# Kernel tuning notes

Hardware: AMD Instinct MI355X
Metric: run time of the kernel (lower is better)

Reference implementation:

```python
import jax, jax.numpy as jnp
import numpy as np
from jax import lax

EPS = 1e-5
DN = ('NCHW', 'OIHW', 'NCHW')


def _bn(x, gamma, beta, mean, var):
    # eval-mode BatchNorm2d over channel dim (axis=1)
    s = gamma / jnp.sqrt(var + EPS)
    return x * s[None, :, None, None] + (beta - mean * s)[None, :, None, None]


def setup_inputs() -> dict:
    key = jax.random.key(0)
    ks = jax.random.split(key, 12)
    B, Cin, C, H, W, NC = 128, 2048, 512, 14, 14, 200
    return {
        'feature': jax.random.normal(ks[0], (B, Cin, H, W), jnp.float32),
        'w_reduce': jax.random.normal(ks[1], (C, Cin, 1, 1), jnp.float32) * 0.02,
        'b_reduce': jax.random.normal(ks[2], (C,), jnp.float32) * 0.02,
        'bn1_gamma': jnp.ones((C,), jnp.float32),
        'bn1_beta': jnp.zeros((C,), jnp.float32),
        'bn1_mean': jax.random.normal(ks[3], (C,), jnp.float32) * 0.02,
        'bn1_var': jax.random.uniform(ks[4], (C,), jnp.float32),
        'w3': jax.random.normal(ks[5], (C, C, 3, 3), jnp.float32) * 0.02,
        'b3': jax.random.normal(ks[6], (C,), jnp.float32) * 0.02,
        'bn2_gamma': jnp.ones((C,), jnp.float32),
        'bn2_beta': jnp.zeros((C,), jnp.float32),
        'bn2_mean': jax.random.normal(ks[7], (C,), jnp.float32) * 0.02,
        'bn2_var': jax.random.uniform(ks[8], (C,), jnp.float32),
        'fc1_w': jax.random.normal(ks[9], (NC, C), jnp.float32) * 0.02,
        'fc1_b': jnp.zeros((NC,), jnp.float32),
        'fc2_w': jax.random.normal(ks[10], (NC, NC), jnp.float32) * 0.02,
        'fc2_b': jnp.zeros((NC,), jnp.float32),
    }


def reference(feature, w_reduce, b_reduce, bn1_gamma, bn1_beta, bn1_mean, bn1_var,
              w3, b3, bn2_gamma, bn2_beta, bn2_mean, bn2_var,
              fc1_w, fc1_b, fc2_w, fc2_b):
    B, _, H, W = feature.shape
    C = w_reduce.shape[0]  # 512
    # reduce: 1x1 conv + BN + ReLU
    f = lax.conv_general_dilated(feature, w_reduce, (1, 1), 'VALID', dimension_numbers=DN)
    f = f + b_reduce[None, :, None, None]
    f = jax.nn.relu(_bn(f, bn1_gamma, bn1_beta, bn1_mean, bn1_var))
    x = f.reshape(B, C, H * W)  # [B, 512, 196]
    # channel affinity + softmax(-xxt) over last dim (= the per-row loop)
    xxt = jnp.einsum('bcn,bdn->bcd', x, x)  # [B, 512, 512]
    a = jax.nn.softmax(-xxt, axis=2)
    y = jnp.einsum('bcd,bdn->bcn', a, x).reshape(B, C, H, W)
    # conv3: 3x3 conv + BN + ReLU + global avg pool
    z = lax.conv_general_dilated(y, w3, (1, 1), 'SAME', dimension_numbers=DN)
    z = z + b3[None, :, None, None]
    z = jax.nn.relu(_bn(z, bn2_gamma, bn2_beta, bn2_mean, bn2_var))
    z = jnp.mean(z, axis=(2, 3))  # [B, 512]
    # fc_channel: Linear -> ReLU -> Linear
    h = jax.nn.relu(z @ fc1_w.T + fc1_b)
    sf = h @ fc2_w.T + fc2_b
    return sf
```

## Files before the change

kernel.cpp:

```cpp
#include <hip/hip_runtime.h>

typedef __attribute__((ext_vector_type(8))) short bf16x8;
typedef __attribute__((ext_vector_type(4))) float f32x4;
typedef __attribute__((ext_vector_type(4))) short short4v;
typedef __attribute__((ext_vector_type(2))) short short2v;

__device__ __forceinline__ unsigned short f2bf(float x){
  unsigned u = __float_as_uint(x);
  return (unsigned short)((u + 0x7FFFu + ((u>>16)&1u)) >> 16);
}
__device__ __forceinline__ float bf2f(unsigned short b){
  return __uint_as_float(((unsigned)b)<<16);
}

typedef const __attribute__((address_space(1))) void* gas_t;
typedef __attribute__((address_space(3))) void* las_t;
__device__ __forceinline__ void gl16(const void* g, void* l){
  __builtin_amdgcn_global_load_lds((gas_t)g, (las_t)l, 16, 0, 0);
}

static constexpr size_t O_FHI  = 0;
static constexpr size_t O_FLO  = 102760448;
static constexpr size_t O_XHI  = 205520896;
static constexpr size_t O_XLO  = 239075328;
static constexpr size_t O_XT   = 272629760;
static constexpr size_t O_AMAT = 301989888;
static constexpr size_t O_WH   = 369098752;
static constexpr size_t O_WL   = 371195904;
static constexpr size_t O_W3B  = 373293056;
static constexpr size_t O_PAR  = 378011648;
static constexpr size_t O_FC1T = 378019840;
static constexpr size_t O_FC2T = 378429440;
static constexpr size_t O_ZBAR = 378589440;

__global__ __launch_bounds__(256) void k_prep(
    const float* wr, unsigned short* wh, unsigned short* wl,
    const float* w3, unsigned short* w3c,
    const float* fc1w, float* fc1T, const float* fc2w, float* fc2T,
    const float* br, const float* g1, const float* be1, const float* m1, const float* v1,
    const float* b3, const float* g2, const float* be2, const float* m2, const float* v2,
    float* par, unsigned short* xhi, unsigned short* xlo){
  int blk = blockIdx.x, t = threadIdx.x;
  if (blk < 4096){
    int idx = blk*256 + t;
    int c = idx >> 11, k = idx & 2047;
    float v = wr[(size_t)c*2048 + k];
    unsigned short h = f2bf(v);
    wh[(size_t)c*2048+k] = h; wl[(size_t)c*2048+k] = f2bf(v - bf2f(h));
  } else if (blk < 13312){
    int i = (blk-4096)*256 + t;
    int co = i / 4608, k = i - co*4608;
    int ci0b = k / 576, r2 = k - ci0b*576;
    int tap = r2 >> 6, cio = r2 & 63;
    w3c[(((size_t)ci0b*9+tap)*512+co)*64+cio] =
        f2bf(w3[((size_t)co*512 + ci0b*64+cio)*9 + tap]);
  } else if (blk < 13712){
    int i = (blk-13312)*256 + t;
    int k = i/200, j = i - k*200;
    fc1T[i] = fc1w[j*512+k];
  } else if (blk < 13869){
    int i = (blk-13712)*256 + t;
    if (i < 40000){ int k = i/200, j = i - k*200; fc2T[i] = fc2w[j*200+k]; }
  } else if (blk < 13871){
    int c = (blk-13869)*256 + t;
    if (c < 512){
      float s1 = g1[c]*rsqrtf(v1[c]+1e-5f);
      par[c] = s1; par[512+c] = (br[c]-m1[c])*s1 + be1[c];
      float s2 = g2[c]*rsqrtf(v2[c]+1e-5f);
      par[1024+c] = s2; par[1536+c] = (b3[c]-m2[c])*s2 + be2[c];
    }
  } else {
    int rr = (blk-13871)*256 + t;
    float4 z = {0.f,0.f,0.f,0.f};
    float4* a = (float4*)(xhi + (size_t)rr*256 + 192);
    float4* bq = (float4*)(xlo + (size_t)rr*256 + 192);
    #pragma unroll
    for (int q=0;q<8;++q){ a[q]=z; bq[q]=z; }
  }
}

__global__ __launch_bounds__(256) void k_featT(const float* __restrict__ feat,
        unsigned short* __restrict__ fhi, unsigned short* __restrict__ flo){
  __shared__ float tile[64][33];
  int b = blockIdx.z;
  int ci0 = blockIdx.y*64, p0 = blockIdx.x*32;
  int t = threadIdx.x;
  int j = t & 31, i0 = t >> 5;
  for (int rep=0; rep<8; ++rep){
    int i = rep*8 + i0;
    int p = p0 + j;
    tile[i][j] = (p<196) ? feat[((size_t)b*2048 + ci0 + i)*196 + p] : 0.f;
  }
  __syncthreads();
  int j2 = t & 31;
  int jj0 = t >> 5;
  for (int rep=0; rep<4; ++rep){
    int jj = rep*8 + jj0;
    int p = p0 + jj;
    if (p < 196){
      float v0 = tile[2*j2][jj], v1 = tile[2*j2+1][jj];
      unsigned short h0 = f2bf(v0), h1 = f2bf(v1);
      unsigned short l0 = f2bf(v0 - bf2f(h0)), l1 = f2bf(v1 - bf2f(h1));
      size_t o = ((size_t)b*196 + p)*2048 + ci0 + 2*j2;
      short2v hv; hv[0]=(short)h0; hv[1]=(short)h1;
      short2v lv; lv[0]=(short)l0; lv[1]=(short)l1;
      *(short2v*)(fhi + o) = hv;
      *(short2v*)(flo + o) = lv;
    }
  }
}

__global__ __launch_bounds__(128, 1) void k_conv1(
    const unsigned short* __restrict__ fhi, const unsigned short* __restrict__ flo,
    const unsigned short* __restrict__ wh,  const unsigned short* __restrict__ wl,
    const float* __restrict__ par,
    unsigned short* __restrict__ xhi, unsigned short* __restrict__ xlo,
    unsigned short* __restrict__ xT){
  __shared__ char lds[65536];
  char* BUF0 = lds;
  char* BUF1 = lds + 32768;
  int lin = blockIdx.x;
  int sz  = (lin&7)*98 + (lin>>3);
  int mt = sz&3;
  int gt = sz>>2;
  int c0 = mt*128;
  size_t g0 = (size_t)gt*128;
  int t = threadIdx.x, lane = t&63, wv = t>>6;
  int fq = (lane>>4)&3, fr = lane&15;
  f32x4 acc[8][4] = {};

  auto STAGE = [&](int it, char* buf){
    #pragma unroll
    for (int jj=0; jj<16; ++jj){
      int arr = jj>>2;
      int g = (jj&3)*128 + t;
      int row = g>>2;
      int cs = ((g&3) ^ ((row>>1)&3))*8;
      const unsigned short* src;
      if (arr==0)      src = wh  + (size_t)(c0+row)*2048 + it*32 + cs;
      else if (arr==1) src = wl  + (size_t)(c0+row)*2048 + it*32 + cs;
      else if (arr==2) src = fhi + (g0+row)*2048 + it*32 + cs;
      else             src = flo + (g0+row)*2048 + it*32 + cs;
      gl16(src, buf + arr*8192 + g*16);
    }
  };

  STAGE(0, BUF0);
  asm volatile("s_waitcnt vmcnt(0)" ::: "memory");
  __builtin_amdgcn_s_barrier();
  __builtin_amdgcn_sched_barrier(0);

  for (int it=0; it<64; ++it){
    char* cur = (it&1) ? BUF1 : BUF0;
    char* nxt = (it&1) ? BUF0 : BUF1;
    if (it < 63) STAGE(it+1, nxt);
    bf16x8 ah[8], al[8];
    #pragma unroll
    for (int m=0;m<8;++m){
      int row = m*16 + fr;
      int off = row*64 + ((fq*16) ^ (((row>>1)&3)<<4));
      ah[m] = *(const bf16x8*)(cur + off);
      al[m] = *(const bf16x8*)(cur + 8192 + off);
    }
    __builtin_amdgcn_s_setprio(1);
    #pragma unroll
    for (int n=0;n<4;++n){
      int row = wv*64 + n*16 + fr;
      int off = row*64 + ((fq*16) ^ (((row>>1)&3)<<4));
      bf16x8 bh = *(const bf16x8*)(cur + 16384 + off);
      bf16x8 bl = *(const bf16x8*)(cur + 24576 + off);
      #pragma unroll
      for (int m=0;m<8;++m){
        acc[m][n] = __builtin_amdgcn_mfma_f32_16x16x32_bf16(ah[m], bh, acc[m][n],0,0,0);
        acc[m][n] = __builtin_amdgcn_mfma_f32_16x16x32_bf16(ah[m], bl, acc[m][n],0,0,0);
        acc[m][n] = __builtin_amdgcn_mfma_f32_16x16x32_bf16(al[m], bh, acc[m][n],0,0,0);
      }
    }
    __builtin_amdgcn_s_setprio(0);
    asm volatile("s_waitcnt vmcnt(0)" ::: "memory");
    __builtin_amdgcn_s_barrier();
    __builtin_amdgcn_sched_barrier(0);
  }

  const float* s1 = par; const float* t1 = par+512;
  for (int m=0;m<8;++m){
    int cb = c0 + m*16 + fq*4;
    float sc[4], sh[4];
    for (int j=0;j<4;++j){ sc[j]=s1[cb+j]; sh[j]=t1[cb+j]; }
    for (int n=0;n<4;++n){
      int gg = (int)g0 + wv*64 + n*16 + fr;
      int b = gg/196, p = gg - b*196;
      unsigned short hs[4];
      for (int j=0;j<4;++j){
        float v = fmaxf(acc[m][n][j]*sc[j]+sh[j], 0.f);
        unsigned short h = f2bf(v);
        hs[j] = h;
        size_t ic = (size_t)b*512 + cb + j;
        xhi[ic*256 + p] = h;
        xlo[ic*256 + p] = f2bf(v - bf2f(h));
      }
      *(short4v*)(xT + ((size_t)b*224 + p)*512 + cb) = *(short4v*)hs;
    }
  }
}

__global__ __launch_bounds__(256) void k_xxt(const unsigned short* __restrict__ xhi,
        const unsigned short* __restrict__ xlo, float* __restrict__ xxt){
  __shared__ char lds[32768];
  char* Als = lds; char* Bls = lds + 16384;
  int lin = blockIdx.x;
  int sz  = (lin&7)*160 + (lin>>3);
  int b = sz/10, sub = sz - b*10;
  unsigned mtp = (3u<<18)|(2u<<16)|(2u<<14)|(1u<<12)|(1u<<10)|(1u<<8)|(0u<<6)|(0u<<4)|(0u<<2)|0u;
  unsigned ntp = (3u<<18)|(3u<<16)|(2u<<14)|(3u<<12)|(2u<<10)|(1u<<8)|(3u<<6)|(2u<<4)|(1u<<2)|0u;
  int mt = (mtp>>(2*sub))&3, nt = (ntp>>(2*sub))&3;
  int c0 = mt*128, d0 = nt*128;
  int t = threadIdx.x, lane = t&63, wid = t>>6, wm = wid&1, wn = wid>>1;
  int fq = lane>>4, fr = lane&15;
  f32x4 acc[4][4] = {};
  for (int it=0; it<12; ++it){
    int seg = it>>2, kk0 = (it&3)*64;
    const unsigned short* As = (seg<2) ? xhi : xlo;
    const unsigned short* Bs = (seg==1) ? xlo : xhi;
    __syncthreads();
    #pragma unroll
    for (int r=0;r<4;++r){
      int L = r*256 + t;
      int row = L>>3, cs = ((L&7)^(row&7))*8;
      gl16(As + ((size_t)b*512 + c0 + row)*256 + kk0 + cs, Als + L*16);
      gl16(Bs + ((size_t)b*512 + d0 + row)*256 + kk0 + cs, Bls + L*16);
    }
    __syncthreads();
    #pragma unroll
    for (int ks=0; ks<2; ++ks){
      int kb = ks*64 + fq*16;
      bf16x8 af[4];
      #pragma unroll
      for (int m=0;m<4;++m){
        int row = wm*64 + m*16 + fr;
        af[m] = *(const bf16x8*)(Als + row*128 + (kb ^ ((row&7)<<4)));
      }
      #pragma unroll
      for (int n=0;n<4;++n){
        int row = wn*64 + n*16 + fr;
        bf16x8 bff = *(const bf16x8*)(Bls + row*128 + (kb ^ ((row&7)<<4)));
        #pragma unroll
        for (int m=0;m<4;++m)
          acc[m][n] = __builtin_amdgcn_mfma_f32_16x16x32_bf16(af[m], bff, acc[m][n],0,0,0);
      }
    }
  }
  for (int m=0;m<4;++m){
    int cb = c0 + wm*64 + m*16 + fq*4;
    for (int n=0;n<4;++n){
      int d = d0 + wn*64 + n*16 + fr;
      *(float4*)(xxt + ((size_t)b*512 + d)*512 + cb) = *(float4*)&acc[m][n];
    }
  }
  if (mt != nt){
    for (int m=0;m<4;++m){
      int cb = c0 + wm*64 + m*16 + fq*4;
      for (int n=0;n<4;++n){
        int d = d0 + wn*64 + n*16 + fr;
        for (int jj=0;jj<4;++jj)
          xxt[((size_t)b*512 + cb + jj)*512 + d] = acc[m][n][jj];
      }
    }
  }
}

__global__ __launch_bounds__(256) void k_softmax(const float* __restrict__ xxt, unsigned short* __restrict__ amat){
  int row = blockIdx.x*4 + (threadIdx.x>>6);
  int lane = threadIdx.x & 63;
  const float* src = xxt + (size_t)row*512 + lane*8;
  float4 v0 = *(const float4*)src;
  float4 v1 = *(const float4*)(src+4);
  float mn = fminf(fminf(fminf(v0.x,v0.y),fminf(v0.z,v0.w)),
                   fminf(fminf(v1.x,v1.y),fminf(v1.z,v1.w)));
  for (int m=32; m; m>>=1) mn = fminf(mn, __shfl_xor(mn, m, 64));
  float e[8];
  e[0]=__expf(mn-v0.x); e[1]=__expf(mn-v0.y); e[2]=__expf(mn-v0.z); e[3]=__expf(mn-v0.w);
  e[4]=__expf(mn-v1.x); e[5]=__expf(mn-v1.y); e[6]=__expf(mn-v1.z); e[7]=__expf(mn-v1.w);
  float s = e[0]+e[1]+e[2]+e[3]+e[4]+e[5]+e[6]+e[7];
  for (int m=32; m; m>>=1) s += __shfl_xor(s, m, 64);
  float inv = 1.f/s;
  short4v p0, p1;
  for (int q=0;q<4;++q) p0[q] = (short)f2bf(e[q]*inv);
  for (int q=0;q<4;++q) p1[q] = (short)f2bf(e[4+q]*inv);
  unsigned short* dst = amat + (size_t)row*512 + lane*8;
  *(short4v*)dst = p0;
  *(short4v*)(dst+4) = p1;
}

__global__ __launch_bounds__(256) void k_pv(const unsigned short* __restrict__ amat,
        const unsigned short* __restrict__ xT, unsigned short* __restrict__ ypad){
  __shared__ char lds[30720];
  char* Als = lds; char* Bls = lds + 16384;
  int lin = blockIdx.x, per = gridDim.x>>3;
  int sz  = (lin&7)*per + (lin>>3);
  int b = sz>>3, sub = sz&7, mt = sub>>1, nt = sub&1;
  int c0 = mt*128, n0 = nt*112;
  int t = threadIdx.x, lane = t&63, wid = t>>6;
  int fq = lane>>4, fr = lane&15;
  {
    int r = t;
    int hi = r>>4, lo2 = r&15;
    if (hi==0||hi==15||lo2==0||lo2==15){
      float4 z = {0.f,0.f,0.f,0.f};
      float4* pz = (float4*)(ypad + (((size_t)b*8 + sub)*256 + r)*64);
      #pragma unroll
      for (int q=0;q<8;++q) pz[q] = z;
    }
  }
  f32x4 acc[2][7] = {};
  for (int it=0; it<8; ++it){
    int k0 = it*64;
    __syncthreads();
    #pragma unroll
    for (int r=0;r<4;++r){
      int L = r*256 + t;
      int row = L>>3, cs = ((L&7)^(row&7))*8;
      gl16(amat + ((size_t)b*512 + c0 + row)*512 + k0 + cs, Als + L*16);
    }
    #pragma unroll
    for (int r=0;r<4;++r){
      int L = r*256 + t;
      if (L < 896){
        int row = L>>3, cs = ((L&7)^(row&7))*8;
        gl16(xT + ((size_t)b*224 + n0 + row)*512 + k0 + cs, Bls + L*16);
      }
    }
    __syncthreads();
    #pragma unroll
    for (int ks=0; ks<2; ++ks){
      int kb = ks*64 + fq*16;
      bf16x8 af[2];
      #pragma unroll
      for (int m=0;m<2;++m){
        int row = wid*32 + m*16 + fr;
        af[m] = *(const bf16x8*)(Als + row*128 + (kb ^ ((row&7)<<4)));
      }
      #pragma unroll
      for (int n=0;n<7;++n){
        int row = n*16 + fr;
        bf16x8 bff = *(const bf16x8*)(Bls + row*128 + (kb ^ ((row&7)<<4)));
        #pragma unroll
        for (int m=0;m<2;++m)
          acc[m][n] = __builtin_amdgcn_mfma_f32_16x16x32_bf16(af[m], bff, acc[m][n],0,0,0);
      }
    }
  }
  for (int m=0;m<2;++m){
    int cb = c0 + wid*32 + m*16 + fq*4;
    int ci0b = cb>>6, cio = cb&63;
    for (int n=0;n<7;++n){
      int p = n0 + n*16 + fr;
      if (p < 196){
        int hh = p/14, wwp = p - hh*14;
        int prow = (hh+1)*16 + (wwp+1);
        short4v pk;
        for (int j=0;j<4;++j) pk[j] = (short)f2bf(acc[m][n][j]);
        *(short4v*)(ypad + (((size_t)b*8 + ci0b)*256 + prow)*64 + cio) = pk;
      }
    }
  }
}

__global__ __launch_bounds__(512, 4) void k_conv3(const unsigned short* __restrict__ ypad,
        const unsigned short* __restrict__ w3c, const float* __restrict__ par,
        float* __restrict__ zbar){
  __shared__ char lds[65536];
  char* WIN = lds;
  char* AB0 = lds + 32768;
  char* AB1 = lds + 49152;
  int bx = blockIdx.x;
  int xcd = bx&7, jj2 = bx>>3;
  int b = xcd*16 + (jj2>>2), cot = jj2&3;
  int c0 = cot*128;
  int t = threadIdx.x, lane = t&63, w = t>>6;
  int wm = w>>1, wn = w&1;
  int fq = lane>>4, fr = lane&15;
  int frB = (fr<14) ? fr : 13;
  bool pok = (fr<14);
  f32x4 acc[2][7] = {};
  for (int ci0=0; ci0<8; ++ci0){
    const unsigned short* wsrc = ypad + ((size_t)(b*8 + ci0)*256)*64;
    #pragma unroll
    for (int r=0;r<4;++r){
      int L = r*512 + t;
      int row = L>>3, cs = ((L&7)^(row&7))*8;
      gl16(wsrc + row*64 + cs, WIN + L*16);
    }
    {
      const unsigned short* asrc = w3c + ((size_t)(ci0*9 + 0)*512 + c0)*64;
      #pragma unroll
      for (int r=0;r<2;++r){
        int L = r*512 + t;
        int row = L>>3, cs = ((L&7)^(row&7))*8;
        gl16(asrc + row*64 + cs, AB0 + L*16);
      }
    }
    __syncthreads();
    for (int tap=0; tap<9; ++tap){
      char* Acur = (tap&1) ? AB1 : AB0;
      char* Anxt = (tap&1) ? AB0 : AB1;
      if (tap < 8){
        const unsigned short* asrc = w3c + ((size_t)(ci0*9 + tap+1)*512 + c0)*64;
        #pragma unroll
        for (int r=0;r<2;++r){
          int L = r*512 + t;
          int row = L>>3, cs = ((L&7)^(row&7))*8;
          gl16(asrc + row*64 + cs, Anxt + L*16);
        }
      }
      int kh = tap/3, kw = tap - kh*3;
      bf16x8 ah[2][2];
      #pragma unroll
      for (int ks=0;ks<2;++ks)
        #pragma unroll
        for (int m=0;m<2;++m){
          int row = wm*32 + m*16 + fr;
          ah[ks][m] = *(const bf16x8*)(Acur + row*128 + (((ks*4+fq)^(row&7))<<4));
        }
      int col = frB + kw;
      __builtin_amdgcn_s_setprio(1);
      #pragma unroll
      for (int n=0;n<7;++n){
        int prow = (wn*7 + n + kh)*16 + col;
        #pragma unroll
        for (int ks=0;ks<2;++ks){
          bf16x8 bf = *(const bf16x8*)(WIN + prow*128 + (((ks*4+fq)^(prow&7))<<4));
          acc[0][n] = __builtin_amdgcn_mfma_f32_16x16x32_bf16(ah[ks][0], bf, acc[0][n],0,0,0);
          acc[1][n] = __builtin_amdgcn_mfma_f32_16x16x32_bf16(ah[ks][1], bf, acc[1][n],0,0,0);
        }
      }
      __builtin_amdgcn_s_setprio(0);
      __syncthreads();
    }
  }
  const float* s2 = par+1024; const float* t2 = par+1536;
  float ps[2][4];
  #pragma unroll
  for (int m=0;m<2;++m){
    int cb = c0 + wm*32 + m*16 + fq*4;
    #pragma unroll
    for (int j=0;j<4;++j){
      float sc = s2[cb+j], sh = t2[cb+j];
      float s = 0.f;
      #pragma unroll
      for (int n=0;n<7;++n)
        s += fmaxf(acc[m][n][j]*sc + sh, 0.f);
      ps[m][j] = pok ? s : 0.f;
    }
  }
  #pragma unroll
  for (int off=1; off<16; off<<=1)
    #pragma unroll
    for (int m=0;m<2;++m)
      #pragma unroll
      for (int j=0;j<4;++j)
        ps[m][j] += __shfl_xor(ps[m][j], off, 64);
  float* part = (float*)lds;
  if (fr == 0){
    #pragma unroll
    for (int m=0;m<2;++m)
      #pragma unroll
      for (int j=0;j<4;++j)
        part[wn*128 + wm*32 + m*16 + fq*4 + j] = ps[m][j];
  }
  __syncthreads();
  if (t < 128)
    zbar[(size_t)b*512 + c0 + t] = part[t] + part[128 + t];
}

__global__ __launch_bounds__(256) void k_fc(const float* __restrict__ zbar,
        const float* __restrict__ fc1T, const float* __restrict__ fc1b,
        const float* __restrict__ fc2T, const float* __restrict__ fc2b,
        float* __restrict__ out){
  __shared__ float zb[512];
  __shared__ float hl[200];
  int b = blockIdx.x, t = threadIdx.x;
  zb[t]     = zbar[(size_t)b*512 + t]       * (1.f/196.f);
  zb[t+256] = zbar[(size_t)b*512 + t + 256] * (1.f/196.f);
  __syncthreads();
  if (t < 200){
    float acc = fc1b[t];
    for (int k=0;k<512;++k) acc += zb[k]*fc1T[k*200+t];
    hl[t] = fmaxf(acc, 0.f);
  }
  __syncthreads();
  if (t < 200){
    float acc = fc2b[t];
    for (int k=0;k<200;++k) acc += hl[k]*fc2T[k*200+t];
    out[(size_t)b*200 + t] = acc;
  }
}

extern "C" void kernel_launch(void* const* d_in, const int* in_sizes, int n_in,
                              void* d_out, int out_size, void* d_ws, size_t ws_size,
                              hipStream_t stream) {
  const float* feature  = (const float*)d_in[0];
  const float* w_reduce = (const float*)d_in[1];
  const float* b_reduce = (const float*)d_in[2];
  const float* g1  = (const float*)d_in[3];
  const float* be1 = (const float*)d_in[4];
  const float* m1  = (const float*)d_in[5];
  const float* v1  = (const float*)d_in[6];
  const float* w3  = (const float*)d_in[7];
  const float* b3  = (const float*)d_in[8];
  const float* g2  = (const float*)d_in[9];
  const float* be2 = (const float*)d_in[10];
  const float* m2  = (const float*)d_in[11];
  const float* v2  = (const float*)d_in[12];
  const float* fc1w = (const float*)d_in[13];
  const float* fc1b = (const float*)d_in[14];
  const float* fc2w = (const float*)d_in[15];
  const float* fc2b = (const float*)d_in[16];

  char* ws = (char*)d_ws;
  unsigned short* fhi  = (unsigned short*)(ws + O_FHI);
  unsigned short* flo  = (unsigned short*)(ws + O_FLO);
  float*          xxt  = (float*)(ws + O_FHI);
  unsigned short* xhi  = (unsigned short*)(ws + O_XHI);
  unsigned short* xlo  = (unsigned short*)(ws + O_XLO);
  unsigned short* ypad = (unsigned short*)(ws + O_XLO);
  unsigned short* xT   = (unsigned short*)(ws + O_XT);
  unsigned short* amat = (unsigned short*)(ws + O_AMAT);
  unsigned short* wh   = (unsigned short*)(ws + O_WH);
  unsigned short* wl   = (unsigned short*)(ws + O_WL);
  unsigned short* w3c  = (unsigned short*)(ws + O_W3B);
  float* par  = (float*)(ws + O_PAR);
  float* fc1T = (float*)(ws + O_FC1T);
  float* fc2T = (float*)(ws + O_FC2T);
  float* zbar = (float*)(ws + O_ZBAR);

  k_prep<<<14127, 256, 0, stream>>>(w_reduce, wh, wl, w3, w3c,
      fc1w, fc1T, fc2w, fc2T,
      b_reduce, g1, be1, m1, v1, b3, g2, be2, m2, v2, par, xhi, xlo);

  k_featT<<<dim3(7,32,128), 256, 0, stream>>>(feature, fhi, flo);
  k_conv1<<<784, 128, 0, stream>>>(fhi, flo, wh, wl, par, xhi, xlo, xT);

  k_xxt<<<1280, 256, 0, stream>>>(xhi, xlo, xxt);
  k_softmax<<<16384, 256, 0, stream>>>(xxt, amat);

  k_pv<<<1024, 256, 0, stream>>>(amat, xT, ypad);
  k_conv3<<<512, 512, 0, stream>>>(ypad, w3c, par, zbar);
  k_fc<<<128, 256, 0, stream>>>(zbar, fc1T, fc1b, fc2T, fc2b, (float*)d_out);
}
```

Baseline: 654.7 us.

## Split conv1 across four waves and conv3 with intra-block K-split reduction

The 1x1 conv GEMM moves from two waves per block (each 128x64) to four waves in a 2x2 grid (each 64x64), doubling the threads per block so more waves share the staged tiles. The 3x3 conv splits the K dimension of each tap across wave pairs, and each wave now covers a 64-row M block. Partial accumulators are combined through LDS in two halves before the BN/ReLU/pool epilogue. This adds more waves to hide latency, at the cost of extra LDS reduction traffic and barriers in conv3 and lower occupancy bounds for conv3.

```diff
diff --git a/kernel.cpp b/kernel.cpp
--- a/kernel.cpp
+++ b/kernel.cpp
@@ -110,7 +110,7 @@
   }
 }
 
-__global__ __launch_bounds__(128, 1) void k_conv1(
+__global__ __launch_bounds__(256, 2) void k_conv1(
     const unsigned short* __restrict__ fhi, const unsigned short* __restrict__ flo,
     const unsigned short* __restrict__ wh,  const unsigned short* __restrict__ wl,
     const float* __restrict__ par,
@@ -125,15 +125,15 @@
   int gt = sz>>2;
   int c0 = mt*128;
   size_t g0 = (size_t)gt*128;
-  int t = threadIdx.x, lane = t&63, wv = t>>6;
-  int fq = (lane>>4)&3, fr = lane&15;
-  f32x4 acc[8][4] = {};
+  int t = threadIdx.x, lane = t&63, wid = t>>6, wm = wid&1, wn = wid>>1;
+  int fq = lane>>4, fr = lane&15;
+  f32x4 acc[4][4] = {};
 
   auto STAGE = [&](int it, char* buf){
     #pragma unroll
-    for (int jj=0; jj<16; ++jj){
-      int arr = jj>>2;
-      int g = (jj&3)*128 + t;
+    for (int jj=0; jj<8; ++jj){
+      int arr = jj>>1;
+      int g = t + ((jj&1)<<8);
       int row = g>>2;
       int cs = ((g&3) ^ ((row>>1)&3))*8;
       const unsigned short* src;
@@ -154,28 +154,30 @@
     char* cur = (it&1) ? BUF1 : BUF0;
     char* nxt = (it&1) ? BUF0 : BUF1;
     if (it < 63) STAGE(it+1, nxt);
-    bf16x8 ah[8], al[8];
-    #pragma unroll
-    for (int m=0;m<8;++m){
-      int row = m*16 + fr;
+    bf16x8 ah[4], al[4], bh[4], bl[4];
+    #pragma unroll
+    for (int m=0;m<4;++m){
+      int row = wm*64 + m*16 + fr;
       int off = row*64 + ((fq*16) ^ (((row>>1)&3)<<4));
       ah[m] = *(const bf16x8*)(cur + off);
       al[m] = *(const bf16x8*)(cur + 8192 + off);
     }
+    #pragma unroll
+    for (int n=0;n<4;++n){
+      int row = wn*64 + n*16 + fr;
+      int off = row*64 + ((fq*16) ^ (((row>>1)&3)<<4));
+      bh[n] = *(const bf16x8*)(cur + 16384 + off);
+      bl[n] = *(const bf16x8*)(cur + 24576 + off);
+    }
     __builtin_amdgcn_s_setprio(1);
     #pragma unroll
-    for (int n=0;n<4;++n){
-      int row = wv*64 + n*16 + fr;
-      int off = row*64 + ((fq*16) ^ (((row>>1)&3)<<4));
-      bf16x8 bh = *(const bf16x8*)(cur + 16384 + off);
-      bf16x8 bl = *(const bf16x8*)(cur + 24576 + off);
-      #pragma unroll
-      for (int m=0;m<8;++m){
-        acc[m][n] = __builtin_amdgcn_mfma_f32_16x16x32_bf16(ah[m], bh, acc[m][n],0,0,0);
-        acc[m][n] = __builtin_amdgcn_mfma_f32_16x16x32_bf16(ah[m], bl, acc[m][n],0,0,0);
-        acc[m][n] = __builtin_amdgcn_mfma_f32_16x16x32_bf16(al[m], bh, acc[m][n],0,0,0);
-      }
-    }
+    for (int n=0;n<4;++n)
+      #pragma unroll
+      for (int m=0;m<4;++m){
+        acc[m][n] = __builtin_amdgcn_mfma_f32_16x16x32_bf16(ah[m], bh[n], acc[m][n],0,0,0);
+        acc[m][n] = __builtin_amdgcn_mfma_f32_16x16x32_bf16(ah[m], bl[n], acc[m][n],0,0,0);
+        acc[m][n] = __builtin_amdgcn_mfma_f32_16x16x32_bf16(al[m], bh[n], acc[m][n],0,0,0);
+      }
     __builtin_amdgcn_s_setprio(0);
     asm volatile("s_waitcnt vmcnt(0)" ::: "memory");
     __builtin_amdgcn_s_barrier();
@@ -183,12 +185,12 @@
   }
 
   const float* s1 = par; const float* t1 = par+512;
-  for (int m=0;m<8;++m){
-    int cb = c0 + m*16 + fq*4;
+  for (int m=0;m<4;++m){
+    int cb = c0 + wm*64 + m*16 + fq*4;
     float sc[4], sh[4];
     for (int j=0;j<4;++j){ sc[j]=s1[cb+j]; sh[j]=t1[cb+j]; }
     for (int n=0;n<4;++n){
-      int gg = (int)g0 + wv*64 + n*16 + fr;
+      int gg = (int)g0 + wn*64 + n*16 + fr;
       int b = gg/196, p = gg - b*196;
       unsigned short hs[4];
       for (int j=0;j<4;++j){
@@ -366,7 +368,7 @@
   }
 }
 
-__global__ __launch_bounds__(512, 4) void k_conv3(const unsigned short* __restrict__ ypad,
+__global__ __launch_bounds__(512, 2) void k_conv3(const unsigned short* __restrict__ ypad,
         const unsigned short* __restrict__ w3c, const float* __restrict__ par,
         float* __restrict__ zbar){
   __shared__ char lds[65536];
@@ -378,11 +380,11 @@
   int b = xcd*16 + (jj2>>2), cot = jj2&3;
   int c0 = cot*128;
   int t = threadIdx.x, lane = t&63, w = t>>6;
-  int wm = w>>1, wn = w&1;
+  int wm = w>>2, wn = (w>>1)&1, wks = w&1;
   int fq = lane>>4, fr = lane&15;
   int frB = (fr<14) ? fr : 13;
   bool pok = (fr<14);
-  f32x4 acc[2][7] = {};
+  f32x4 acc[4][7] = {};
   for (int ci0=0; ci0<8; ++ci0){
     const unsigned short* wsrc = ypad + ((size_t)(b*8 + ci0)*256)*64;
     #pragma unroll
@@ -414,59 +416,78 @@
         }
       }
       int kh = tap/3, kw = tap - kh*3;
-      bf16x8 ah[2][2];
-      #pragma unroll
-      for (int ks=0;ks<2;++ks)
-        #pragma unroll
-        for (int m=0;m<2;++m){
-          int row = wm*32 + m*16 + fr;
-          ah[ks][m] = *(const bf16x8*)(Acur + row*128 + (((ks*4+fq)^(row&7))<<4));
-        }
+      bf16x8 ah[4];
+      #pragma unroll
+      for (int m=0;m<4;++m){
+        int row = wm*64 + m*16 + fr;
+        ah[m] = *(const bf16x8*)(Acur + row*128 + (((wks*4+fq)^(row&7))<<4));
+      }
       int col = frB + kw;
       __builtin_amdgcn_s_setprio(1);
       #pragma unroll
       for (int n=0;n<7;++n){
         int prow = (wn*7 + n + kh)*16 + col;
-        #pragma unroll
-        for (int ks=0;ks<2;++ks){
-          bf16x8 bf = *(const bf16x8*)(WIN + prow*128 + (((ks*4+fq)^(prow&7))<<4));
-          acc[0][n] = __builtin_amdgcn_mfma_f32_16x16x32_bf16(ah[ks][0], bf, acc[0][n],0,0,0);
-          acc[1][n] = __builtin_amdgcn_mfma_f32_16x16x32_bf16(ah[ks][1], bf, acc[1][n],0,0,0);
-        }
+        bf16x8 bf = *(const bf16x8*)(WIN + prow*128 + (((wks*4+fq)^(prow&7))<<4));
+        #pragma unroll
+        for (int m=0;m<4;++m)
+          acc[m][n] = __builtin_amdgcn_mfma_f32_16x16x32_bf16(ah[m], bf, acc[m][n],0,0,0);
       }
       __builtin_amdgcn_s_setprio(0);
       __syncthreads();
     }
   }
+  #pragma unroll
+  for (int half=0; half<2; ++half){
+    if (wks){
+      #pragma unroll
+      for (int m2=0;m2<2;++m2)
+        #pragma unroll
+        for (int n=0;n<7;++n)
+          *(f32x4*)(lds + (((size_t)((wm*2+wn)*14 + m2*7 + n))*64 + lane)*16) = acc[half*2+m2][n];
+    }
+    __syncthreads();
+    if (!wks){
+      #pragma unroll
+      for (int m2=0;m2<2;++m2)
+        #pragma unroll
+        for (int n=0;n<7;++n){
+          f32x4 o = *(const f32x4*)(lds + (((size_t)((wm*2+wn)*14 + m2*7 + n))*64 + lane)*16);
+          acc[half*2+m2][n] += o;
+        }
+    }
+    __syncthreads();
+  }
   const float* s2 = par+1024; const float* t2 = par+1536;
-  float ps[2][4];
-  #pragma unroll
-  for (int m=0;m<2;++m){
-    int cb = c0 + wm*32 + m*16 + fq*4;
-    #pragma unroll
-    for (int j=0;j<4;++j){
-      float sc = s2[cb+j], sh = t2[cb+j];
-      float s = 0.f;
-      #pragma unroll
-      for (int n=0;n<7;++n)
-        s += fmaxf(acc[m][n][j]*sc + sh, 0.f);
-      ps[m][j] = pok ? s : 0.f;
-    }
-  }
-  #pragma unroll
-  for (int off=1; off<16; off<<=1)
-    #pragma unroll
-    for (int m=0;m<2;++m)
+  float ps[4][4];
+  if (!wks){
+    #pragma unroll
+    for (int m=0;m<4;++m){
+      int cb = c0 + wm*64 + m*16 + fq*4;
+      #pragma unroll
+      for (int j=0;j<4;++j){
+        float sc = s2[cb+j], sh = t2[cb+j];
+        float s = 0.f;
+        #pragma unroll
+        for (int n=0;n<7;++n)
+          s += fmaxf(acc[m][n][j]*sc + sh, 0.f);
+        ps[m][j] = pok ? s : 0.f;
+      }
+    }
+    #pragma unroll
+    for (int off=1; off<16; off<<=1)
+      #pragma unroll
+      for (int m=0;m<4;++m)
+        #pragma unroll
+        for (int j=0;j<4;++j)
+          ps[m][j] += __shfl_xor(ps[m][j], off, 64);
+  }
+  float* part = (float*)lds;
+  if (!wks && fr == 0){
+    #pragma unroll
+    for (int m=0;m<4;++m)
       #pragma unroll
       for (int j=0;j<4;++j)
-        ps[m][j] += __shfl_xor(ps[m][j], off, 64);
-  float* part = (float*)lds;
-  if (fr == 0){
-    #pragma unroll
-    for (int m=0;m<2;++m)
-      #pragma unroll
-      for (int j=0;j<4;++j)
-        part[wn*128 + wm*32 + m*16 + fq*4 + j] = ps[m][j];
+        part[wn*128 + wm*64 + m*16 + fq*4 + j] = ps[m][j];
   }
   __syncthreads();
   if (t < 128)
@@ -539,7 +560,7 @@
       b_reduce, g1, be1, m1, v1, b3, g2, be2, m2, v2, par, xhi, xlo);
 
   k_featT<<<dim3(7,32,128), 256, 0, stream>>>(feature, fhi, flo);
-  k_conv1<<<784, 128, 0, stream>>>(fhi, flo, wh, wl, par, xhi, xlo, xT);
+  k_conv1<<<784, 256, 0, stream>>>(fhi, flo, wh, wl, par, xhi, xlo, xT);
 
   k_xxt<<<1280, 256, 0, stream>>>(xhi, xlo, xxt);
   k_softmax<<<16384, 256, 0, stream>>>(xxt, amat);
```

Measured after the change: 593.3 us. 9.4% less time.
